# Optimization experiments

Hardware: AMD Instinct MI355X
Metric: run time of the kernel (lower is better)

Reference implementation:

```python
import jax, jax.numpy as jnp
import numpy as np

N_NODES = 10000
N_EDGES = 640000
D_IN = 128
D_OUT = 128


def setup_inputs() -> dict:
    key = jax.random.key(0)
    k1, k2, k3, k4 = jax.random.split(key, 4)
    x = jax.random.normal(k1, (N_NODES, D_IN), dtype=jnp.float32)
    # PyG GCNConv weight: [dim_out, dim_in] (glorot)
    W = jax.random.normal(k2, (D_OUT, D_IN), dtype=jnp.float32) * (1.0 / np.sqrt(D_IN))
    b = jnp.zeros((D_OUT,), dtype=jnp.float32)
    edge_weight = jax.random.uniform(k3, (N_EDGES,), dtype=jnp.float32)
    edge_index = jax.random.randint(k4, (2, N_EDGES), 0, N_NODES, dtype=jnp.int32)
    return {"x": x, "W": W, "b": b, "edge_weight": edge_weight, "edge_index": edge_index}


def reference(x, W, b, edge_weight, edge_index):
    N = x.shape[0]
    # --- add self loops (fill weight = 1.0), PyG default ---
    loops = jnp.arange(N, dtype=edge_index.dtype)
    src = jnp.concatenate([edge_index[0], loops])
    dst = jnp.concatenate([edge_index[1], loops])
    ew = jnp.concatenate([edge_weight, jnp.ones((N,), dtype=edge_weight.dtype)])
    # --- symmetric GCN normalization: deg from target index ---
    deg = jax.ops.segment_sum(ew, dst, num_segments=N)
    dinv = jnp.where(deg > 0, jax.lax.rsqrt(deg), 0.0)
    norm = dinv[src] * ew * dinv[dst]  # [E+N]
    # --- linear transform then gather-scale-scatter aggregation ---
    h = x @ W.T  # [N, D_OUT]
    msgs = h[src] * norm[:, None]  # [E+N, D_OUT]
    out = jax.ops.segment_sum(msgs, dst, num_segments=N)
    return out + b
```

## Files before the change

kernel.cpp:

```cpp
#include <hip/hip_runtime.h>

#define N_NODES 10000
#define N_EDGES 640000
#define D 128
#define CAP 128

typedef unsigned long long ull;
typedef unsigned short u16;
typedef unsigned int u32;

#define CHUNKS 512
#define EPC 1250
#define NR 500
#define RW 20
#define CELLCAP 20
#define GEMM_NPB 32
#define GEMM_BLOCKS ((N_NODES + GEMM_NPB - 1) / GEMM_NPB)
#define SMEM_K1 16384
#define EWFX 262144.0f
#define EWM  0x1ffffffu

__device__ __forceinline__ u16 f2bf(float f) {
    unsigned u = __float_as_uint(f);
    unsigned r = (u + 0x7fffu + ((u >> 16) & 1u)) >> 16;
    return (u16)r;
}


__global__ void __launch_bounds__(256) k_bucket(
    const int* __restrict__ src, const int* __restrict__ dst,
    const float* __restrict__ ew, const float* __restrict__ x,
    const float* __restrict__ W, u16* __restrict__ h_bf,
    ull* __restrict__ ebuf)
{
    extern __shared__ char smem[];
    const int t = threadIdx.x;

    if (blockIdx.x < CHUNKS) {
        u32* rcnt = (u32*)smem;
        for (int i = t; i < NR; i += 256) rcnt[i] = 0;
        __syncthreads();

        const int e0 = blockIdx.x * EPC;
        #pragma unroll
        for (int i = 0; i < 5; ++i) {
            int idx = i * 256 + t;
            if (idx < EPC) {
                int e = e0 + idx;
                int d = dst[e];
                int s = src[e];
                float w = ew[e];
                int r = d / RW;
                int bin = d - r * RW;
                u32 slot = atomicAdd(&rcnt[r], 1u);
                if (slot < CELLCAP) {
                    ebuf[((size_t)r * CHUNKS + blockIdx.x) * CELLCAP + slot] =
                        ((ull)__float_as_uint(w) << 32) | ((u32)s << 5) | (u32)bin;
                }
            }
        }
        __syncthreads();

        for (int i = t; i < NR; i += 256) {
            u32 slot = rcnt[i];
            if (slot < CELLCAP)
                ebuf[((size_t)i * CHUNKS + blockIdx.x) * CELLCAP + slot] = 31ull;
        }
    } else {
        float* xs = (float*)smem;
        const int node0 = (blockIdx.x - CHUNKS) * GEMM_NPB;
        const int col = t & 127;
        const int half = t >> 7;

        #pragma unroll
        for (int r = 0; r < 16; ++r) {
            int row = half * 16 + r;
            int n = node0 + row;
            xs[row * D + col] = (n < N_NODES) ? x[n * D + col] : 0.0f;
        }
        __syncthreads();

        float acc[16];
        #pragma unroll
        for (int r = 0; r < 16; ++r) acc[r] = 0.0f;

        const float4* Wrow = (const float4*)&W[col * D];
        const float* xbase = &xs[half * 16 * D];
        for (int k4 = 0; k4 < D / 4; ++k4) {
            float4 w = Wrow[k4];
            int k = k4 * 4;
            #pragma unroll
            for (int r = 0; r < 16; ++r) {
                acc[r] += xbase[r * D + k + 0] * w.x;
                acc[r] += xbase[r * D + k + 1] * w.y;
                acc[r] += xbase[r * D + k + 2] * w.z;
                acc[r] += xbase[r * D + k + 3] * w.w;
            }
        }
        #pragma unroll
        for (int r = 0; r < 16; ++r) {
            int n = node0 + half * 16 + r;
            if (n < N_NODES) h_bf[n * D + col] = f2bf(acc[r]);
        }
    }
}


#define REC(s) (((s) & 1) ? (((ull)rr[(s) >> 1].w << 32) | (ull)rr[(s) >> 1].z) \
                          : (((ull)rr[(s) >> 1].y << 32) | (ull)rr[(s) >> 1].x))

__global__ void __launch_bounds__(512) k_csr(
    const ull* __restrict__ ebuf, u32* __restrict__ gpacked,
    float* __restrict__ dinv, ull* __restrict__ csr)
{
    __shared__ u32 bcnt[RW];
    const int t = threadIdx.x;
    const int r = blockIdx.x;

    if (t < RW) bcnt[t] = 0;

    uint4 rr[CELLCAP / 2];
    const uint4* pb = (const uint4*)(ebuf + ((size_t)r * CHUNKS + t) * CELLCAP);
    #pragma unroll
    for (int i = 0; i < CELLCAP / 2; ++i) rr[i] = pb[i];
    __syncthreads();

    int cnt = CELLCAP;
    #pragma unroll
    for (int s = CELLCAP - 1; s >= 0; --s)
        if (((u32)REC(s) & 31u) == 31u) cnt = s;

    #pragma unroll
    for (int s = 0; s < CELLCAP; ++s) {
        if (s < cnt) {
            ull v = REC(s);
            u32 lo = (u32)v;
            int bin = (int)(lo & 31u);
            u32 srcn = lo >> 5;
            u32 wb = (u32)(v >> 32);
            float w = __uint_as_float(wb);
            u32 add = (1u << 25) | (u32)(w * EWFX);
            u32 old = atomicAdd(&bcnt[bin], add);
            int pos = (int)(old >> 25);
            if (pos < CAP) {
                int dstg = r * RW + bin;
                csr[(size_t)dstg * CAP + pos] = ((ull)wb << 32) | srcn;
            }
        }
    }
    __syncthreads();

    if (t < RW) {
        int n = r * RW + t;
        u32 v = bcnt[t];
        gpacked[n] = v;
        dinv[n] = rsqrtf(1.0f + (float)(v & EWM) * 0x1p-18f);
    }
}


#define AGG_NPB 4

__global__ void __launch_bounds__(256) k_agg(
    const u32* __restrict__ gpacked, const float* __restrict__ dinv,
    const ull* __restrict__ csr, const u16* __restrict__ h_bf,
    const float* __restrict__ b, float* __restrict__ out)
{
    const int wid  = threadIdx.x >> 6;
    const int lane = threadIdx.x & 63;
    const int n = blockIdx.x * AGG_NPB + wid;

    __shared__ ull sm[AGG_NPB][CAP];

    const int deg = (int)(gpacked[n] >> 25);
    const float dn = dinv[n];
    const ull* bucket = csr + (size_t)n * CAP;

    #pragma unroll
    for (int r = 0; r < 2; ++r) {
        int j = r * 64 + lane;
        if (j < deg) {
            ull v = bucket[j];
            int s = (int)(u32)(v & 0xffffffffu);
            float w = __uint_as_float((u32)(v >> 32));
            float nm = dinv[s] * w * dn;
            sm[wid][j] = ((ull)__float_as_uint(nm) << 32) | (u32)s;
        }
    }
    __syncthreads();

    float acc0 = 0.0f, acc1 = 0.0f;
    const ull* smw = sm[wid];
    #pragma unroll 4
    for (int j = 0; j < deg; ++j) {
        ull v = smw[j];
        int s = (int)(u32)v;
        float nm = __uint_as_float((u32)(v >> 32));
        u32 hc = *(const u32*)(h_bf + (size_t)s * D + lane * 2);
        acc0 += __uint_as_float(hc << 16) * nm;
        acc1 += __uint_as_float(hc & 0xffff0000u) * nm;
    }

    float s2 = dn * dn;
    u32 hs = *(const u32*)(h_bf + (size_t)n * D + lane * 2);
    acc0 += __uint_as_float(hs << 16) * s2;
    acc1 += __uint_as_float(hs & 0xffff0000u) * s2;
    float2 bb = *(const float2*)(b + lane * 2);
    float2 o;
    o.x = acc0 + bb.x;
    o.y = acc1 + bb.y;
    *(float2*)(out + (size_t)n * D + lane * 2) = o;
}


extern "C" void kernel_launch(void* const* d_in, const int* in_sizes, int n_in,
                              void* d_out, int out_size, void* d_ws, size_t ws_size,
                              hipStream_t stream) {
    const float* x  = (const float*)d_in[0];
    const float* W  = (const float*)d_in[1];
    const float* b  = (const float*)d_in[2];
    const float* ew = (const float*)d_in[3];
    const int* ei   = (const int*)d_in[4];
    const int* src = ei;
    const int* dst = ei + N_EDGES;
    float* out = (float*)d_out;

    char* ws = (char*)d_ws;
    u32*   gpacked = (u32*)(ws);
    float* dinv    = (float*)(ws + 40000);
    u16*   h_bf    = (u16*)(ws + 80000);
    ull*   csr     = (ull*)(ws + 2640000);
    ull*   ebuf    = (ull*)(ws + 12880000);

    k_bucket<<<CHUNKS + GEMM_BLOCKS, 256, SMEM_K1, stream>>>(
        src, dst, ew, x, W, h_bf, ebuf);
    k_csr<<<NR, 512, 0, stream>>>(ebuf, gpacked, dinv, csr);
    k_agg<<<N_NODES / AGG_NPB, 256, 0, stream>>>(gpacked, dinv, csr, h_bf, b, out);
}
```

Baseline: 121.8 us.

## Sort edges per chunk in shared memory and emit compact records with offsets

```diff
diff --git a/kernel.cpp b/kernel.cpp
--- a/kernel.cpp
+++ b/kernel.cpp
@@ -13,7 +13,6 @@
 #define EPC 1250
 #define NR 500
 #define RW 20
-#define CELLCAP 20
 #define GEMM_NPB 32
 #define GEMM_BLOCKS ((N_NODES + GEMM_NPB - 1) / GEMM_NPB)
 #define SMEM_K1 16384
@@ -31,20 +30,26 @@
     const int* __restrict__ src, const int* __restrict__ dst,
     const float* __restrict__ ew, const float* __restrict__ x,
     const float* __restrict__ W, u16* __restrict__ h_bf,
-    ull* __restrict__ ebuf)
+    ull* __restrict__ grecs, u32* __restrict__ offs)
 {
     extern __shared__ char smem[];
     const int t = threadIdx.x;
 
     if (blockIdx.x < CHUNKS) {
-        u32* rcnt = (u32*)smem;
-        for (int i = t; i < NR; i += 256) rcnt[i] = 0;
+        u32* rcnt   = (u32*)smem;
+        u32* ping   = (u32*)(smem + 2048);
+        u32* pong   = (u32*)(smem + 4096);
+        ull* sorted = (ull*)(smem + 6144);
+
+        for (int i = t; i < 512; i += 256) rcnt[i] = 0;
         __syncthreads();
 
         const int e0 = blockIdx.x * EPC;
+        u32 rs[5]; ull rec[5];
         #pragma unroll
         for (int i = 0; i < 5; ++i) {
             int idx = i * 256 + t;
+            rs[i] = 0xffffffffu;
             if (idx < EPC) {
                 int e = e0 + idx;
                 int d = dst[e];
@@ -53,18 +58,39 @@
                 int r = d / RW;
                 int bin = d - r * RW;
                 u32 slot = atomicAdd(&rcnt[r], 1u);
-                if (slot < CELLCAP) {
-                    ebuf[((size_t)r * CHUNKS + blockIdx.x) * CELLCAP + slot] =
-                        ((ull)__float_as_uint(w) << 32) | ((u32)s << 5) | (u32)bin;
-                }
+                rs[i] = ((u32)r << 11) | slot;
+                rec[i] = ((ull)__float_as_uint(w) << 32) | ((u32)s << 5) | (u32)bin;
             }
         }
         __syncthreads();
 
-        for (int i = t; i < NR; i += 256) {
-            u32 slot = rcnt[i];
-            if (slot < CELLCAP)
-                ebuf[((size_t)i * CHUNKS + blockIdx.x) * CELLCAP + slot] = 31ull;
+        u32* a = ping; u32* bq = pong;
+        for (int i = t; i < 512; i += 256) a[i] = rcnt[i];
+        __syncthreads();
+        for (int dd = 1; dd < 512; dd <<= 1) {
+            for (int i = t; i < 512; i += 256)
+                bq[i] = a[i] + ((i >= dd) ? a[i - dd] : 0u);
+            __syncthreads();
+            u32* tmp = a; a = bq; bq = tmp;
+        }
+
+        #pragma unroll
+        for (int i = 0; i < 5; ++i) {
+            if (rs[i] != 0xffffffffu) {
+                int r = (int)(rs[i] >> 11);
+                int slot = (int)(rs[i] & 2047u);
+                sorted[a[r] - rcnt[r] + slot] = rec[i];
+            }
+        }
+        __syncthreads();
+
+        {
+            const uint4* sp = (const uint4*)sorted;
+            uint4* gp = (uint4*)(grecs + (size_t)blockIdx.x * EPC);
+            for (int i = t; i < EPC / 2; i += 256) gp[i] = sp[i];
+            u32* ob = offs + (size_t)blockIdx.x * 512;
+            for (int i = t; i < NR; i += 256) ob[i] = a[i] - rcnt[i];
+            if (t == 0) ob[NR] = EPC;
         }
     } else {
         float* xs = (float*)smem;
@@ -106,12 +132,9 @@
 }
 
 
-#define REC(s) (((s) & 1) ? (((ull)rr[(s) >> 1].w << 32) | (ull)rr[(s) >> 1].z) \
-                          : (((ull)rr[(s) >> 1].y << 32) | (ull)rr[(s) >> 1].x))
-
 __global__ void __launch_bounds__(512) k_csr(
-    const ull* __restrict__ ebuf, u32* __restrict__ gpacked,
-    float* __restrict__ dinv, ull* __restrict__ csr)
+    const ull* __restrict__ grecs, const u32* __restrict__ offs,
+    u32* __restrict__ gpacked, float* __restrict__ dinv, ull* __restrict__ csr)
 {
     __shared__ u32 bcnt[RW];
     const int t = threadIdx.x;
@@ -119,33 +142,29 @@
 
     if (t < RW) bcnt[t] = 0;
 
-    uint4 rr[CELLCAP / 2];
-    const uint4* pb = (const uint4*)(ebuf + ((size_t)r * CHUNKS + t) * CELLCAP);
-    #pragma unroll
-    for (int i = 0; i < CELLCAP / 2; ++i) rr[i] = pb[i];
+    const u32* ob = offs + (size_t)t * 512;
+    u32 o0 = ob[r], o1 = ob[r + 1];
+    if (o0 > EPC) o0 = EPC;
+    if (o1 > EPC) o1 = EPC;
+    int cnt = (int)o1 - (int)o0;
+    if (cnt < 0) cnt = 0;
+    if (cnt > 64) cnt = 64;
     __syncthreads();
 
-    int cnt = CELLCAP;
-    #pragma unroll
-    for (int s = CELLCAP - 1; s >= 0; --s)
-        if (((u32)REC(s) & 31u) == 31u) cnt = s;
-
-    #pragma unroll
-    for (int s = 0; s < CELLCAP; ++s) {
-        if (s < cnt) {
-            ull v = REC(s);
-            u32 lo = (u32)v;
-            int bin = (int)(lo & 31u);
-            u32 srcn = lo >> 5;
-            u32 wb = (u32)(v >> 32);
-            float w = __uint_as_float(wb);
-            u32 add = (1u << 25) | (u32)(w * EWFX);
-            u32 old = atomicAdd(&bcnt[bin], add);
-            int pos = (int)(old >> 25);
-            if (pos < CAP) {
-                int dstg = r * RW + bin;
-                csr[(size_t)dstg * CAP + pos] = ((ull)wb << 32) | srcn;
-            }
+    const ull* seg = grecs + (size_t)t * EPC + o0;
+    for (int j = 0; j < cnt; ++j) {
+        ull v = seg[j];
+        u32 lo = (u32)v;
+        int bin = (int)(lo & 31u);
+        u32 srcn = lo >> 5;
+        u32 wb = (u32)(v >> 32);
+        float w = __uint_as_float(wb);
+        u32 add = (1u << 25) | (u32)(w * EWFX);
+        u32 old = atomicAdd(&bcnt[bin], add);
+        int pos = (int)(old >> 25);
+        if (pos < CAP) {
+            int dstg = r * RW + bin;
+            csr[(size_t)dstg * CAP + pos] = ((ull)wb << 32) | srcn;
         }
     }
     __syncthreads();
@@ -230,10 +249,11 @@
     float* dinv    = (float*)(ws + 40000);
     u16*   h_bf    = (u16*)(ws + 80000);
     ull*   csr     = (ull*)(ws + 2640000);
-    ull*   ebuf    = (ull*)(ws + 12880000);
+    ull*   grecs   = (ull*)(ws + 12880000);
+    u32*   offs    = (u32*)(ws + 18000000);
 
     k_bucket<<<CHUNKS + GEMM_BLOCKS, 256, SMEM_K1, stream>>>(
-        src, dst, ew, x, W, h_bf, ebuf);
-    k_csr<<<NR, 512, 0, stream>>>(ebuf, gpacked, dinv, csr);
+        src, dst, ew, x, W, h_bf, grecs, offs);
+    k_csr<<<NR, 512, 0, stream>>>(grecs, offs, gpacked, dinv, csr);
     k_agg<<<N_NODES / AGG_NPB, 256, 0, stream>>>(gpacked, dinv, csr, h_bf, b, out);
 }
```

Result: faster. 116.9 us (-4.0%).
